# Kernel optimization log

Measured on AMD Instinct MI355X. Metric: run time of the kernel, lower is better.

## Reference

```python
import jax, jax.numpy as jnp
import numpy as np

D_K = 64
D_MODEL = 1024
N_HEADS = 16


def setup_inputs() -> dict:
    key = jax.random.key(0)
    ks = jax.random.split(key, 9)
    B, S = 2, 2048
    scale = 1.0 / np.sqrt(D_MODEL)
    inp = {
        "x": jax.random.normal(ks[0], (B, S, D_MODEL), dtype=jnp.float32),
        "w_q": jax.random.normal(ks[1], (D_MODEL, N_HEADS * D_K), dtype=jnp.float32) * scale,
        "b_q": jnp.zeros((N_HEADS * D_K,), dtype=jnp.float32),
        "w_k": jax.random.normal(ks[2], (D_MODEL, N_HEADS * D_K), dtype=jnp.float32) * scale,
        "b_k": jnp.zeros((N_HEADS * D_K,), dtype=jnp.float32),
        "w_v": jax.random.normal(ks[3], (D_MODEL, N_HEADS * D_K), dtype=jnp.float32) * scale,
        "b_v": jnp.zeros((N_HEADS * D_K,), dtype=jnp.float32),
        "w_o": jax.random.normal(ks[4], (N_HEADS * D_K, D_MODEL), dtype=jnp.float32) * scale,
        "b_o": jnp.zeros((D_MODEL,), dtype=jnp.float32),
    }
    return inp


def reference(x, w_q, b_q, w_k, b_k, w_v, b_v, w_o, b_o):
    B, S, _ = x.shape
    H, Dk = N_HEADS, D_K

    def split_heads(m):  # [B,S,H*Dk] -> [B,H,S,Dk]
        return m.reshape(B, S, H, Dk).transpose(0, 2, 1, 3)

    Q = split_heads(x @ w_q + b_q)
    K = split_heads(x @ w_k + b_k)
    V = split_heads(x @ w_v + b_v)

    scores = jnp.einsum("bhsd,bhtd->bhst", Q, K) / jnp.sqrt(jnp.float32(Dk))
    probs = jax.nn.softmax(scores, axis=-1)
    attn = jnp.einsum("bhst,bhtd->bhsd", probs, V)  # [B,H,S,Dk]
    attn = attn.transpose(0, 2, 1, 3).reshape(B, S, H * Dk)
    return attn @ w_o + b_o
```

## Files before the change

### kernel.cpp

```cpp
#include <hip/hip_runtime.h>
#include <math.h>

#define D_MODELc 1024
#define N_HEADSc 16
#define D_Kc     64
#define B_SZc    2
#define S_LENc   2048
#define NTOKc    (B_SZc * S_LENc)

using half8  = __attribute__((ext_vector_type(8))) _Float16;
using half4  = __attribute__((ext_vector_type(4))) _Float16;
using fp16x2 = __attribute__((ext_vector_type(2))) __fp16;
using float4v = __attribute__((ext_vector_type(4))) float;

__global__ __launch_bounds__(256) void cvt_all(
    const float* __restrict__ x,
    const float* __restrict__ W0, const float* __restrict__ W1,
    const float* __restrict__ W2, const float* __restrict__ W3,
    _Float16* __restrict__ wout, _Float16* __restrict__ xout)
{
    __shared__ float T[32][33];
    const int z = blockIdx.z;
    const int t = threadIdx.x;

    if (z == 4) {
        const int bid = blockIdx.y * 32 + blockIdx.x;
        #pragma unroll
        for (int c = 0; c < 2; ++c) {
            const int i = bid * 512 + c * 256 + t;
            float4v a = ((const float4v*)x)[2 * i];
            float4v b = ((const float4v*)x)[2 * i + 1];
            half8 h;
            h[0] = (_Float16)a[0]; h[1] = (_Float16)a[1];
            h[2] = (_Float16)a[2]; h[3] = (_Float16)a[3];
            h[4] = (_Float16)b[0]; h[5] = (_Float16)b[1];
            h[6] = (_Float16)b[2]; h[7] = (_Float16)b[3];
            ((half8*)xout)[i] = h;
        }
        return;
    }

    const float* W = (z == 0) ? W0 : (z == 1) ? W1 : (z == 2) ? W2 : W3;
    _Float16* O = wout + (size_t)z * 1024 * 1024;

    const int k0 = blockIdx.x * 32;
    const int n0 = blockIdx.y * 32;
    {
        const int r = t >> 3, c4 = (t & 7) * 4;
        float4v v = *(const float4v*)(W + (size_t)(k0 + r) * 1024 + n0 + c4);
        T[r][c4 + 0] = v[0]; T[r][c4 + 1] = v[1];
        T[r][c4 + 2] = v[2]; T[r][c4 + 3] = v[3];
    }
    __syncthreads();
    {
        const int rn = t >> 3, ck4 = (t & 7) * 4;
        half4 h;
        h[0] = (_Float16)T[ck4 + 0][rn];
        h[1] = (_Float16)T[ck4 + 1][rn];
        h[2] = (_Float16)T[ck4 + 2][rn];
        h[3] = (_Float16)T[ck4 + 3][rn];
        *(half4*)(O + (size_t)(n0 + rn) * 1024 + k0 + ck4) = h;
    }
}

__global__ __launch_bounds__(256) void gemm_qkv(
    const _Float16* __restrict__ A, const _Float16* __restrict__ BtAll,
    const float* __restrict__ bias0, const float* __restrict__ bias1,
    const float* __restrict__ bias2, _Float16* __restrict__ Cout)
{
    __shared__ _Float16 Als[128 * 32];
    __shared__ _Float16 Bls[128 * 32];

    constexpr int K = 1024;
    const int tid = threadIdx.x;
    const int m0  = blockIdx.x * 128;
    const int n0  = blockIdx.y * 128;
    const int z   = blockIdx.z;

    const _Float16* Bt  = BtAll + (size_t)z * 1024 * 1024;
    const float* bias   = (z == 0) ? bias0 : (z == 1) ? bias1 : bias2;
    const float qscale  = (z == 0) ? 0.18033688011112042f : 1.0f;

    const int wave = tid >> 6, lane = tid & 63;
    const int wr = wave >> 1, wc = wave & 1;
    const int quad = lane >> 4, l16 = lane & 15;

    float4v acc[4][4];
    #pragma unroll
    for (int i = 0; i < 4; ++i)
        #pragma unroll
        for (int j = 0; j < 4; ++j)
            acc[i][j] = (float4v){0.f, 0.f, 0.f, 0.f};

    for (int k0 = 0; k0 < K; k0 += 32) {
        #pragma unroll
        for (int c = 0; c < 2; ++c) {
            const int i   = c * 256 + tid;
            const int row = i >> 2, kc = i & 3;
            const _Float16* ga = A  + (size_t)(m0 + row) * K + k0 + kc * 8;
            const _Float16* gb = Bt + (size_t)(n0 + row) * K + k0 + kc * 8;
            __builtin_amdgcn_global_load_lds(
                (const __attribute__((address_space(1))) void*)ga,
                (__attribute__((address_space(3))) void*)(Als + i * 8), 16, 0, 0);
            __builtin_amdgcn_global_load_lds(
                (const __attribute__((address_space(1))) void*)gb,
                (__attribute__((address_space(3))) void*)(Bls + i * 8), 16, 0, 0);
        }
        __syncthreads();

        half8 af[4], bf[4];
        #pragma unroll
        for (int i = 0; i < 4; ++i)
            af[i] = *(const half8*)(Als + (wr * 64 + i * 16 + l16) * 32 + quad * 8);
        #pragma unroll
        for (int j = 0; j < 4; ++j)
            bf[j] = *(const half8*)(Bls + (wc * 64 + j * 16 + l16) * 32 + quad * 8);
        #pragma unroll
        for (int i = 0; i < 4; ++i)
            #pragma unroll
            for (int j = 0; j < 4; ++j)
                acc[i][j] = __builtin_amdgcn_mfma_f32_16x16x32_f16(
                    af[i], bf[j], acc[i][j], 0, 0, 0);
        __syncthreads();
    }

    if (z != 2) {
        #pragma unroll
        for (int i = 0; i < 4; ++i) {
            const int rbase = m0 + wr * 64 + i * 16 + quad * 4;
            #pragma unroll
            for (int j = 0; j < 4; ++j) {
                const int col = n0 + wc * 64 + j * 16 + l16;
                const float bv = bias[col];
                #pragma unroll
                for (int r = 0; r < 4; ++r) {
                    const float v = (acc[i][j][r] + bv) * qscale;
                    const int n = rbase + r;
                    const int b = n >> 11, s = n & 2047;
                    const int h = col >> 6, d = col & 63;
                    _Float16* C = Cout + (size_t)z * NTOKc * D_MODELc;
                    C[(((size_t)(b * N_HEADSc + h)) * S_LENc + s) * D_Kc + d] =
                        (_Float16)v;
                }
            }
        }
    } else {
        #pragma unroll
        for (int i = 0; i < 4; ++i) {
            const int rbase = m0 + wr * 64 + i * 16 + quad * 4;
            const int b = rbase >> 11, s0 = rbase & 2047;
            #pragma unroll
            for (int j = 0; j < 4; ++j) {
                const int col = n0 + wc * 64 + j * 16 + l16;
                const float bv = bias[col];
                const int h = col >> 6, d = col & 63;
                half4 hv;
                #pragma unroll
                for (int r = 0; r < 4; ++r)
                    hv[r] = (_Float16)(acc[i][j][r] + bv);
                _Float16* C = Cout + (size_t)2 * NTOKc * D_MODELc;
                *(half4*)(C + (((size_t)(b * N_HEADSc + h)) * D_Kc + d) *
                          S_LENc + s0) = hv;
            }
        }
    }
}

__global__ __launch_bounds__(256) void gemm_out(
    const _Float16* __restrict__ A, const _Float16* __restrict__ Bt,
    const float* __restrict__ bias, float* __restrict__ C)
{
    __shared__ _Float16 Als[64 * 32];
    __shared__ _Float16 Bls[128 * 32];

    constexpr int K = 1024;
    const int tid = threadIdx.x;
    const int m0  = blockIdx.x * 64;
    const int n0  = blockIdx.y * 128;

    const int wave = tid >> 6, lane = tid & 63;
    const int wr = wave >> 1, wc = wave & 1;
    const int quad = lane >> 4, l16 = lane & 15;

    float4v acc[2][4];
    #pragma unroll
    for (int i = 0; i < 2; ++i)
        #pragma unroll
        for (int j = 0; j < 4; ++j)
            acc[i][j] = (float4v){0.f, 0.f, 0.f, 0.f};

    for (int k0 = 0; k0 < K; k0 += 32) {
        {
            const int row = tid >> 2, kc = tid & 3;
            __builtin_amdgcn_global_load_lds(
                (const __attribute__((address_space(1))) void*)
                    (A + (size_t)(m0 + row) * K + k0 + kc * 8),
                (__attribute__((address_space(3))) void*)(Als + tid * 8), 16, 0, 0);
        }
        #pragma unroll
        for (int c = 0; c < 2; ++c) {
            const int i = c * 256 + tid;
            const int row = i >> 2, kc = i & 3;
            __builtin_amdgcn_global_load_lds(
                (const __attribute__((address_space(1))) void*)
                    (Bt + (size_t)(n0 + row) * K + k0 + kc * 8),
                (__attribute__((address_space(3))) void*)(Bls + i * 8), 16, 0, 0);
        }
        __syncthreads();

        half8 af[2], bf[4];
        #pragma unroll
        for (int i = 0; i < 2; ++i)
            af[i] = *(const half8*)(Als + (wr * 32 + i * 16 + l16) * 32 + quad * 8);
        #pragma unroll
        for (int j = 0; j < 4; ++j)
            bf[j] = *(const half8*)(Bls + (wc * 64 + j * 16 + l16) * 32 + quad * 8);
        #pragma unroll
        for (int i = 0; i < 2; ++i)
            #pragma unroll
            for (int j = 0; j < 4; ++j)
                acc[i][j] = __builtin_amdgcn_mfma_f32_16x16x32_f16(
                    af[i], bf[j], acc[i][j], 0, 0, 0);
        __syncthreads();
    }

    #pragma unroll
    for (int i = 0; i < 2; ++i) {
        const int rbase = m0 + wr * 32 + i * 16 + quad * 4;
        #pragma unroll
        for (int j = 0; j < 4; ++j) {
            const int col = n0 + wc * 64 + j * 16 + l16;
            const float bv = bias[col];
            #pragma unroll
            for (int r = 0; r < 4; ++r)
                C[(size_t)(rbase + r) * 1024 + col] = acc[i][j][r] + bv;
        }
    }
}

__global__ __launch_bounds__(256) void attn_mfma(
    const _Float16* __restrict__ Qb, const _Float16* __restrict__ Kb,
    const _Float16* __restrict__ Vtg, _Float16* __restrict__ Op,
    float* __restrict__ Lp)
{
    constexpr int PS = 72;
    __shared__ _Float16 Ks[64 * PS];
    __shared__ _Float16 Vt[64 * PS];
    __shared__ _Float16 Ps[128 * PS];

    const int tid  = threadIdx.x;
    const int wv   = tid >> 6;
    const int lane = tid & 63;
    const int quad = lane >> 4;
    const int l16  = lane & 15;

    const int q0 = blockIdx.x * 128;
    const int bh = blockIdx.y;
    const int sp = blockIdx.z;
    const int kb = sp * (S_LENc / 2);
    const int kend = kb + S_LENc / 2;

    const _Float16* Qsl = Qb  + (size_t)bh * S_LENc * D_Kc;
    const _Float16* Ksl = Kb  + (size_t)bh * S_LENc * D_Kc;
    const _Float16* Vsl = Vtg + (size_t)bh * S_LENc * D_Kc;

    half8 aq[2][2];
    #pragma unroll
    for (int qf = 0; qf < 2; ++qf) {
        const int row = q0 + wv * 32 + qf * 16 + l16;
        aq[qf][0] = *(const half8*)(Qsl + (size_t)row * 64 + quad * 8);
        aq[qf][1] = *(const half8*)(Qsl + (size_t)row * 64 + 32 + quad * 8);
    }

    float4v O[2][4];
    #pragma unroll
    for (int qf = 0; qf < 2; ++qf)
        #pragma unroll
        for (int nt = 0; nt < 4; ++nt)
            O[qf][nt] = (float4v){0.f, 0.f, 0.f, 0.f};
    float lr[2] = {0.f, 0.f};

    const int sr = tid >> 2;
    const int sg = (tid & 3) * 16;

    half8 k0 = *(const half8*)(Ksl + (size_t)(kb + sr) * 64 + sg);
    half8 k1 = *(const half8*)(Ksl + (size_t)(kb + sr) * 64 + sg + 8);
    half8 v0 = *(const half8*)(Vsl + (size_t)sr * S_LENc + kb + sg);
    half8 v1 = *(const half8*)(Vsl + (size_t)sr * S_LENc + kb + sg + 8);

    for (int t0 = kb; t0 < kend; t0 += 64) {
        __syncthreads();
        *(half8*)(Ks + sr * PS + sg)     = k0;
        *(half8*)(Ks + sr * PS + sg + 8) = k1;
        *(half8*)(Vt + sr * PS + sg)     = v0;
        *(half8*)(Vt + sr * PS + sg + 8) = v1;
        __syncthreads();

        const int tn = (t0 + 64 < kend) ? t0 + 64 : kb;
        k0 = *(const half8*)(Ksl + (size_t)(tn + sr) * 64 + sg);
        k1 = *(const half8*)(Ksl + (size_t)(tn + sr) * 64 + sg + 8);
        v0 = *(const half8*)(Vsl + (size_t)sr * S_LENc + tn + sg);
        v1 = *(const half8*)(Vsl + (size_t)sr * S_LENc + tn + sg + 8);

        half8 kf[4][2];
        #pragma unroll
        for (int nt = 0; nt < 4; ++nt) {
            kf[nt][0] = *(const half8*)(Ks + (nt * 16 + l16) * PS + quad * 8);
            kf[nt][1] = *(const half8*)(Ks + (nt * 16 + l16) * PS + 32 + quad * 8);
        }

        #pragma unroll
        for (int qf = 0; qf < 2; ++qf) {
            float4v st[4];
            #pragma unroll
            for (int nt = 0; nt < 4; ++nt) {
                st[nt] = __builtin_amdgcn_mfma_f32_16x16x32_f16(
                    kf[nt][0], aq[qf][0], (float4v){0.f, 0.f, 0.f, 0.f}, 0, 0, 0);
                st[nt] = __builtin_amdgcn_mfma_f32_16x16x32_f16(
                    kf[nt][1], aq[qf][1], st[nt], 0, 0, 0);
            }
            float ls = 0.f;
            #pragma unroll
            for (int nt = 0; nt < 4; ++nt) {
                const float p0 = __builtin_amdgcn_exp2f(fminf(st[nt][0], 15.5f));
                const float p1 = __builtin_amdgcn_exp2f(fminf(st[nt][1], 15.5f));
                const float p2 = __builtin_amdgcn_exp2f(fminf(st[nt][2], 15.5f));
                const float p3 = __builtin_amdgcn_exp2f(fminf(st[nt][3], 15.5f));
                ls += (p0 + p1) + (p2 + p3);
                union { fp16x2 h2[2]; half4 h4; } u;
                u.h2[0] = __builtin_amdgcn_cvt_pkrtz(p0, p1);
                u.h2[1] = __builtin_amdgcn_cvt_pkrtz(p2, p3);
                *(half4*)(Ps + (wv * 32 + qf * 16 + l16) * PS +
                          nt * 16 + quad * 4) = u.h4;
            }
            lr[qf] += ls;
        }

        half8 bvv[4][2];
        #pragma unroll
        for (int nt = 0; nt < 4; ++nt) {
            bvv[nt][0] = *(const half8*)(Vt + (nt * 16 + l16) * PS + quad * 8);
            bvv[nt][1] = *(const half8*)(Vt + (nt * 16 + l16) * PS + 32 + quad * 8);
        }
        #pragma unroll
        for (int qf = 0; qf < 2; ++qf) {
            half8 ap0 = *(const half8*)(Ps + (wv * 32 + qf * 16 + l16) * PS + quad * 8);
            half8 ap1 = *(const half8*)(Ps + (wv * 32 + qf * 16 + l16) * PS + 32 + quad * 8);
            #pragma unroll
            for (int nt = 0; nt < 4; ++nt) {
                O[qf][nt] = __builtin_amdgcn_mfma_f32_16x16x32_f16(
                    ap0, bvv[nt][0], O[qf][nt], 0, 0, 0);
                O[qf][nt] = __builtin_amdgcn_mfma_f32_16x16x32_f16(
                    ap1, bvv[nt][1], O[qf][nt], 0, 0, 0);
            }
        }
    }

    const size_t qgb = (size_t)bh * S_LENc;
    #pragma unroll
    for (int qf = 0; qf < 2; ++qf) {
        float t = lr[qf];
        t += __shfl_xor(t, 16, 64);
        t += __shfl_xor(t, 32, 64);
        if (quad == 0)
            Lp[(size_t)sp * 65536 + qgb + q0 + wv * 32 + qf * 16 + l16] = t;
        #pragma unroll
        for (int r = 0; r < 4; ++r) {
            const int q = q0 + wv * 32 + qf * 16 + quad * 4 + r;
            _Float16* dst = Op + ((size_t)sp * 65536 + qgb + q) * 64;
            #pragma unroll
            for (int nt = 0; nt < 4; ++nt)
                dst[nt * 16 + l16] = (_Float16)O[qf][nt][r];
        }
    }
}

__global__ __launch_bounds__(256) void attn_combine(
    const _Float16* __restrict__ Op, const float* __restrict__ Lp,
    _Float16* __restrict__ Ab)
{
    const int i  = blockIdx.x * 256 + threadIdx.x;
    const int e0 = i * 8;
    const int qg = e0 >> 6;
    const int d0 = e0 & 63;
    const int bh = qg >> 11, q = qg & 2047;
    const int b  = bh >> 4,  h = bh & 15;

    const float inv = 1.0f / (Lp[qg] + Lp[65536 + qg]);
    half8 o0 = *(const half8*)(Op + (size_t)qg * 64 + d0);
    half8 o1 = *(const half8*)(Op + ((size_t)65536 + qg) * 64 + d0);
    half8 hv;
    #pragma unroll
    for (int j = 0; j < 8; ++j)
        hv[j] = (_Float16)(((float)o0[j] + (float)o1[j]) * inv);
    *(half8*)(Ab + ((size_t)(b * S_LENc + q)) * 1024 + h * 64 + d0) = hv;
}

extern "C" void kernel_launch(void* const* d_in, const int* in_sizes, int n_in,
                              void* d_out, int out_size, void* d_ws, size_t ws_size,
                              hipStream_t stream)
{
    const float* x  = (const float*)d_in[0];
    const float* wq = (const float*)d_in[1];
    const float* bq = (const float*)d_in[2];
    const float* wk = (const float*)d_in[3];
    const float* bk = (const float*)d_in[4];
    const float* wv = (const float*)d_in[5];
    const float* bv = (const float*)d_in[6];
    const float* wo = (const float*)d_in[7];
    const float* bo = (const float*)d_in[8];
    float* out = (float*)d_out;

    const size_t M1 = 1024 * 1024;
    const size_t M4 = 4 * M1;
    _Float16* xh = (_Float16*)d_ws;
    _Float16* wh = xh + M4;
    _Float16* Qh = wh + M4;
    _Float16* Oph = Qh + 3 * M4;
    float*    Lp  = (float*)(Oph + 2 * M4);
    _Float16* Ah = xh;

    cvt_all<<<dim3(32, 32, 5), dim3(256), 0, stream>>>(
        x, wq, wk, wv, wo, wh, xh);
    gemm_qkv<<<dim3(NTOKc / 128, D_MODELc / 128, 3), dim3(256), 0, stream>>>(
        xh, wh, bq, bk, bv, Qh);
    attn_mfma<<<dim3(S_LENc / 128, B_SZc * N_HEADSc, 2), dim3(256), 0, stream>>>(
        Qh, Qh + M4, Qh + 2 * M4, Oph, Lp);
    attn_combine<<<dim3(NTOKc * D_MODELc / 8 / 256), dim3(256), 0, stream>>>(
        Oph, Lp, Ah);
    gemm_out<<<dim3(NTOKc / 64, D_MODELc / 128), dim3(256), 0, stream>>>(
        Ah, wh + 3 * M1, bo, out);
}
```

Baseline: 217.5 us.

## Double K-step per barrier in GEMMs and drop register prefetch in attention

Both projection GEMMs now stage a 64-wide K slice per iteration, split into two 32-wide LDS halves, so each pair of barriers covers twice as many MFMAs and the loop runs half as many iterations. Shared memory per block doubles, which may lower occupancy. The attention kernel removes the software prefetch of the next K/V tile into registers and loads the current tile at the top of each iteration instead. That frees registers but exposes global load latency before the LDS store.

New measurement: 206.1 us. 5.2% less time.

```diff
diff --git a/kernel.cpp b/kernel.cpp
--- a/kernel.cpp
+++ b/kernel.cpp
@@ -68,8 +68,8 @@
     const float* __restrict__ bias0, const float* __restrict__ bias1,
     const float* __restrict__ bias2, _Float16* __restrict__ Cout)
 {
-    __shared__ _Float16 Als[128 * 32];
-    __shared__ _Float16 Bls[128 * 32];
+    __shared__ _Float16 Als[2][128 * 32];
+    __shared__ _Float16 Bls[2][128 * 32];
 
     constexpr int K = 1024;
     const int tid = threadIdx.x;
@@ -92,35 +92,49 @@
         for (int j = 0; j < 4; ++j)
             acc[i][j] = (float4v){0.f, 0.f, 0.f, 0.f};
 
-    for (int k0 = 0; k0 < K; k0 += 32) {
+    for (int k0 = 0; k0 < K; k0 += 64) {
         #pragma unroll
         for (int c = 0; c < 2; ++c) {
             const int i   = c * 256 + tid;
             const int row = i >> 2, kc = i & 3;
-            const _Float16* ga = A  + (size_t)(m0 + row) * K + k0 + kc * 8;
-            const _Float16* gb = Bt + (size_t)(n0 + row) * K + k0 + kc * 8;
-            __builtin_amdgcn_global_load_lds(
-                (const __attribute__((address_space(1))) void*)ga,
-                (__attribute__((address_space(3))) void*)(Als + i * 8), 16, 0, 0);
-            __builtin_amdgcn_global_load_lds(
-                (const __attribute__((address_space(1))) void*)gb,
-                (__attribute__((address_space(3))) void*)(Bls + i * 8), 16, 0, 0);
-        }
-        __syncthreads();
-
-        half8 af[4], bf[4];
+            #pragma unroll
+            for (int h = 0; h < 2; ++h) {
+                __builtin_amdgcn_global_load_lds(
+                    (const __attribute__((address_space(1))) void*)
+                        (A + (size_t)(m0 + row) * K + k0 + h * 32 + kc * 8),
+                    (__attribute__((address_space(3))) void*)(Als[h] + i * 8),
+                    16, 0, 0);
+                __builtin_amdgcn_global_load_lds(
+                    (const __attribute__((address_space(1))) void*)
+                        (Bt + (size_t)(n0 + row) * K + k0 + h * 32 + kc * 8),
+                    (__attribute__((address_space(3))) void*)(Bls[h] + i * 8),
+                    16, 0, 0);
+            }
+        }
+        __syncthreads();
+
+        half8 af[4][2], bf[4][2];
+        #pragma unroll
+        for (int i = 0; i < 4; ++i) {
+            const int r = (wr * 64 + i * 16 + l16) * 32 + quad * 8;
+            af[i][0] = *(const half8*)(Als[0] + r);
+            af[i][1] = *(const half8*)(Als[1] + r);
+        }
+        #pragma unroll
+        for (int j = 0; j < 4; ++j) {
+            const int r = (wc * 64 + j * 16 + l16) * 32 + quad * 8;
+            bf[j][0] = *(const half8*)(Bls[0] + r);
+            bf[j][1] = *(const half8*)(Bls[1] + r);
+        }
         #pragma unroll
         for (int i = 0; i < 4; ++i)
-            af[i] = *(const half8*)(Als + (wr * 64 + i * 16 + l16) * 32 + quad * 8);
-        #pragma unroll
-        for (int j = 0; j < 4; ++j)
-            bf[j] = *(const half8*)(Bls + (wc * 64 + j * 16 + l16) * 32 + quad * 8);
-        #pragma unroll
-        for (int i = 0; i < 4; ++i)
-            #pragma unroll
-            for (int j = 0; j < 4; ++j)
+            #pragma unroll
+            for (int j = 0; j < 4; ++j) {
                 acc[i][j] = __builtin_amdgcn_mfma_f32_16x16x32_f16(
-                    af[i], bf[j], acc[i][j], 0, 0, 0);
+                    af[i][0], bf[j][0], acc[i][j], 0, 0, 0);
+                acc[i][j] = __builtin_amdgcn_mfma_f32_16x16x32_f16(
+                    af[i][1], bf[j][1], acc[i][j], 0, 0, 0);
+            }
         __syncthreads();
     }
 
@@ -170,8 +184,8 @@
     const _Float16* __restrict__ A, const _Float16* __restrict__ Bt,
     const float* __restrict__ bias, float* __restrict__ C)
 {
-    __shared__ _Float16 Als[64 * 32];
-    __shared__ _Float16 Bls[128 * 32];
+    __shared__ _Float16 Als[2][64 * 32];
+    __shared__ _Float16 Bls[2][128 * 32];
 
     constexpr int K = 1024;
     const int tid = threadIdx.x;
@@ -189,38 +203,53 @@
         for (int j = 0; j < 4; ++j)
             acc[i][j] = (float4v){0.f, 0.f, 0.f, 0.f};
 
-    for (int k0 = 0; k0 < K; k0 += 32) {
+    for (int k0 = 0; k0 < K; k0 += 64) {
         {
             const int row = tid >> 2, kc = tid & 3;
-            __builtin_amdgcn_global_load_lds(
-                (const __attribute__((address_space(1))) void*)
-                    (A + (size_t)(m0 + row) * K + k0 + kc * 8),
-                (__attribute__((address_space(3))) void*)(Als + tid * 8), 16, 0, 0);
+            #pragma unroll
+            for (int h = 0; h < 2; ++h)
+                __builtin_amdgcn_global_load_lds(
+                    (const __attribute__((address_space(1))) void*)
+                        (A + (size_t)(m0 + row) * K + k0 + h * 32 + kc * 8),
+                    (__attribute__((address_space(3))) void*)(Als[h] + tid * 8),
+                    16, 0, 0);
         }
         #pragma unroll
         for (int c = 0; c < 2; ++c) {
             const int i = c * 256 + tid;
             const int row = i >> 2, kc = i & 3;
-            __builtin_amdgcn_global_load_lds(
-                (const __attribute__((address_space(1))) void*)
-                    (Bt + (size_t)(n0 + row) * K + k0 + kc * 8),
-                (__attribute__((address_space(3))) void*)(Bls + i * 8), 16, 0, 0);
-        }
-        __syncthreads();
-
-        half8 af[2], bf[4];
+            #pragma unroll
+            for (int h = 0; h < 2; ++h)
+                __builtin_amdgcn_global_load_lds(
+                    (const __attribute__((address_space(1))) void*)
+                        (Bt + (size_t)(n0 + row) * K + k0 + h * 32 + kc * 8),
+                    (__attribute__((address_space(3))) void*)(Bls[h] + i * 8),
+                    16, 0, 0);
+        }
+        __syncthreads();
+
+        half8 af[2][2], bf[4][2];
+        #pragma unroll
+        for (int i = 0; i < 2; ++i) {
+            const int r = (wr * 32 + i * 16 + l16) * 32 + quad * 8;
+            af[i][0] = *(const half8*)(Als[0] + r);
+            af[i][1] = *(const half8*)(Als[1] + r);
+        }
+        #pragma unroll
+        for (int j = 0; j < 4; ++j) {
+            const int r = (wc * 64 + j * 16 + l16) * 32 + quad * 8;
+            bf[j][0] = *(const half8*)(Bls[0] + r);
+            bf[j][1] = *(const half8*)(Bls[1] + r);
+        }
         #pragma unroll
         for (int i = 0; i < 2; ++i)
-            af[i] = *(const half8*)(Als + (wr * 32 + i * 16 + l16) * 32 + quad * 8);
-        #pragma unroll
-        for (int j = 0; j < 4; ++j)
-            bf[j] = *(const half8*)(Bls + (wc * 64 + j * 16 + l16) * 32 + quad * 8);
-        #pragma unroll
-        for (int i = 0; i < 2; ++i)
-            #pragma unroll
-            for (int j = 0; j < 4; ++j)
+            #pragma unroll
+            for (int j = 0; j < 4; ++j) {
                 acc[i][j] = __builtin_amdgcn_mfma_f32_16x16x32_f16(
-                    af[i], bf[j], acc[i][j], 0, 0, 0);
+                    af[i][0], bf[j][0], acc[i][j], 0, 0, 0);
+                acc[i][j] = __builtin_amdgcn_mfma_f32_16x16x32_f16(
+                    af[i][1], bf[j][1], acc[i][j], 0, 0, 0);
+            }
         __syncthreads();
     }
 
@@ -283,24 +312,17 @@
     const int sr = tid >> 2;
     const int sg = (tid & 3) * 16;
 
-    half8 k0 = *(const half8*)(Ksl + (size_t)(kb + sr) * 64 + sg);
-    half8 k1 = *(const half8*)(Ksl + (size_t)(kb + sr) * 64 + sg + 8);
-    half8 v0 = *(const half8*)(Vsl + (size_t)sr * S_LENc + kb + sg);
-    half8 v1 = *(const half8*)(Vsl + (size_t)sr * S_LENc + kb + sg + 8);
-
     for (int t0 = kb; t0 < kend; t0 += 64) {
+        half8 k0 = *(const half8*)(Ksl + (size_t)(t0 + sr) * 64 + sg);
+        half8 k1 = *(const half8*)(Ksl + (size_t)(t0 + sr) * 64 + sg + 8);
+        half8 v0 = *(const half8*)(Vsl + (size_t)sr * S_LENc + t0 + sg);
+        half8 v1 = *(const half8*)(Vsl + (size_t)sr * S_LENc + t0 + sg + 8);
         __syncthreads();
         *(half8*)(Ks + sr * PS + sg)     = k0;
         *(half8*)(Ks + sr * PS + sg + 8) = k1;
         *(half8*)(Vt + sr * PS + sg)     = v0;
         *(half8*)(Vt + sr * PS + sg + 8) = v1;
         __syncthreads();
-
-        const int tn = (t0 + 64 < kend) ? t0 + 64 : kb;
-        k0 = *(const half8*)(Ksl + (size_t)(tn + sr) * 64 + sg);
-        k1 = *(const half8*)(Ksl + (size_t)(tn + sr) * 64 + sg + 8);
-        v0 = *(const half8*)(Vsl + (size_t)sr * S_LENc + tn + sg);
-        v1 = *(const half8*)(Vsl + (size_t)sr * S_LENc + tn + sg + 8);
 
         half8 kf[4][2];
         #pragma unroll
```
